# Kernel optimization log

Measured on AMD Instinct MI355X. Metric: run time of the kernel, lower is better.

The kernel has to match this reference:

```python
import jax, jax.numpy as jnp
import numpy as np

DIM = 1024
NUM_HEADS = 16
NUM_KV_HEADS = 4
HEAD_DIM = DIM // NUM_HEADS
KV_DIM = NUM_KV_HEADS * HEAD_DIM
PARTIAL_ROPE_DIM = 32
ROPE_BASE = 10000.0
LORA_RANK = 4
NUM_LORA_STEPS = 2
LORA_SCALE = 1.0
B, S = 2, 2048


def _rms_norm(x):
    eps = jnp.asarray(jnp.finfo(x.dtype).eps, x.dtype)
    return x * jax.lax.rsqrt(jnp.mean(x * x, axis=-1, keepdims=True) + eps)


def _rope_cos_sin(seq_len, dtype):
    half = PARTIAL_ROPE_DIM // 2
    inv_freq = 1.0 / (ROPE_BASE ** (jnp.arange(0, PARTIAL_ROPE_DIM, 2, dtype=jnp.float32) / PARTIAL_ROPE_DIM))
    t = jnp.arange(seq_len, dtype=jnp.float32)
    freqs = jnp.outer(t, inv_freq)  # [S, half]
    return jnp.cos(freqs).astype(dtype), jnp.sin(freqs).astype(dtype)


def _apply_rope_partial(x, cos, sin):
    # x: [B, H, S, D]; rotate first PARTIAL_ROPE_DIM dims, pass the rest.
    half = PARTIAL_ROPE_DIM // 2
    x1 = x[..., :half]
    x2 = x[..., half:PARTIAL_ROPE_DIM]
    xp = x[..., PARTIAL_ROPE_DIM:]
    c = cos[None, None, :, :]
    s = sin[None, None, :, :]
    return jnp.concatenate([x1 * c + x2 * s, -x1 * s + x2 * c, xp], axis=-1)


def setup_inputs() -> dict:
    key = jax.random.key(0)
    ks = jax.random.split(key, 12)
    std = 0.02
    return {
        "x": jax.random.normal(ks[0], (B, S, DIM), jnp.float32),
        "Wq": jax.random.normal(ks[1], (DIM, DIM), jnp.float32) * std,
        "Wk": jax.random.normal(ks[2], (KV_DIM, DIM), jnp.float32) * std,
        "Wv": jax.random.normal(ks[3], (KV_DIM, DIM), jnp.float32) * std,
        "Wproj": jax.random.normal(ks[4], (DIM, DIM), jnp.float32) * std,
        "q_gain": jnp.full((NUM_HEADS,), 1.0, jnp.float32),
        "lora_A_q": jax.random.normal(ks[5], (NUM_LORA_STEPS, LORA_RANK, DIM), jnp.float32) * std,
        "lora_B_q": jax.random.normal(ks[6], (NUM_LORA_STEPS, DIM, LORA_RANK), jnp.float32) * std,
        "lora_A_v": jax.random.normal(ks[7], (NUM_LORA_STEPS, LORA_RANK, DIM), jnp.float32) * std,
        "lora_B_v": jax.random.normal(ks[8], (NUM_LORA_STEPS, KV_DIM, LORA_RANK), jnp.float32) * std,
        "step_idx": 0,
    }


def reference(x, Wq, Wk, Wv, Wproj, q_gain, lora_A_q, lora_B_q, lora_A_v, lora_B_v, step_idx):
    bsz, seqlen, dim = x.shape
    q = x @ Wq.T
    v = x @ Wv.T
    if 0 <= step_idx < NUM_LORA_STEPS:
        q = q + LORA_SCALE * ((x @ lora_A_q[step_idx].T) @ lora_B_q[step_idx].T)
        v = v + LORA_SCALE * ((x @ lora_A_v[step_idx].T) @ lora_B_v[step_idx].T)
    k = x @ Wk.T

    q = q.reshape(bsz, seqlen, NUM_HEADS, HEAD_DIM).transpose(0, 2, 1, 3)      # [B,H,S,D]
    k = k.reshape(bsz, seqlen, NUM_KV_HEADS, HEAD_DIM).transpose(0, 2, 1, 3)   # [B,Hkv,S,D]
    v = v.reshape(bsz, seqlen, NUM_KV_HEADS, HEAD_DIM).transpose(0, 2, 1, 3)

    q = _rms_norm(q)
    k = _rms_norm(k)

    cos, sin = _rope_cos_sin(seqlen, q.dtype)
    q = _apply_rope_partial(q, cos, sin)
    k = _apply_rope_partial(k, cos, sin)

    q = q * q_gain.astype(q.dtype)[None, :, None, None]

    # GQA causal SDPA
    groups = NUM_HEADS // NUM_KV_HEADS
    qg = q.reshape(bsz, NUM_KV_HEADS, groups, seqlen, HEAD_DIM)
    scale = 1.0 / np.sqrt(HEAD_DIM)
    scores = jnp.einsum('bkgsd,bktd->bkgst', qg, k) * scale  # [B,Hkv,G,S,S]
    causal = jnp.tril(jnp.ones((seqlen, seqlen), bool))
    scores = jnp.where(causal[None, None, None], scores, jnp.asarray(-jnp.inf, scores.dtype))
    attn = jax.nn.softmax(scores, axis=-1)
    y = jnp.einsum('bkgst,bktd->bkgsd', attn, v)
    y = y.reshape(bsz, NUM_HEADS, seqlen, HEAD_DIM).transpose(0, 2, 1, 3).reshape(bsz, seqlen, dim)
    return y @ Wproj.T
```

## Files before the change

kernel.cpp:

```cpp
#include <hip/hip_runtime.h>
#include <hip/hip_bf16.h>
#include <stdint.h>

#define DIM 1024
#define NH 16
#define NKV 4
#define HD 64
#define SEQ 2048
#define BATCH 2
#define RANK 4
#define NSTEPS 2

#define XN      4194304
#define WQ_END  5242880
#define WK_END  5505024
#define WV_END  5767168
#define CVT_BLOCKS 6656
#define LORA_BLOCKS 1024

typedef unsigned short u16;
typedef unsigned int u32;
typedef __attribute__((ext_vector_type(8))) __bf16 bf16x8;
typedef __attribute__((ext_vector_type(4))) float f32x4;

__device__ __forceinline__ float bf2f(u16 v) {
    u32 u = ((u32)v) << 16;
    return __builtin_bit_cast(float, u);
}
__device__ __forceinline__ u16 f2bf(float f) {
    u32 u = __builtin_bit_cast(u32, f);
    u32 r = (u + 0x7fffu + ((u >> 16) & 1u)) >> 16;
    return (u16)r;
}
__device__ __forceinline__ u32 pk2(float a, float b) {
    return (u32)f2bf(a) | ((u32)f2bf(b) << 16);
}
__device__ __forceinline__ u32 pk2t(float a, float b) {
    return __builtin_amdgcn_perm(__builtin_bit_cast(u32, b),
                                 __builtin_bit_cast(u32, a), 0x07060302u);
}
__device__ __forceinline__ void glds16(const u16* g, u16* l) {
    __builtin_amdgcn_global_load_lds(
        (const __attribute__((address_space(1))) u32*)g,
        (__attribute__((address_space(3))) u32*)l, 16, 0, 0);
}

__global__ __launch_bounds__(256) void k_prep(
    const float* __restrict__ x, const float* __restrict__ Wq,
    const float* __restrict__ Wk, const float* __restrict__ Wv,
    const float* __restrict__ Wp, u16* __restrict__ dst,
    const float* __restrict__ Aq, const float* __restrict__ Av,
    const int* __restrict__ step_p, float* __restrict__ tq, float* __restrict__ tv)
{
    int bx = blockIdx.x;
    if (bx < CVT_BLOCKS) {
        int e = (bx * 256 + threadIdx.x) * 4;
        const float* src;
        if (e < XN)          src = x  + e;
        else if (e < WQ_END) src = Wq + (e - XN);
        else if (e < WK_END) src = Wk + (e - WQ_END);
        else if (e < WV_END) src = Wv + (e - WK_END);
        else                 src = Wp + (e - WV_END);
        float4 v = *(const float4*)src;
        *(uint2*)(dst + e) = make_uint2(pk2(v.x, v.y), pk2(v.z, v.w));
        return;
    }
    int wave = ((bx - CVT_BLOCKS) * 256 + threadIdx.x) >> 6;
    int lane = threadIdx.x & 63;
    int step = step_p[0];
    int valid = (step >= 0 && step < NSTEPS);
    int sc = valid ? step : 0;
    const float* xr = x + wave * DIM + lane * 16;
    float xf[16];
#pragma unroll
    for (int q = 0; q < 4; q++) {
        float4 v4 = *(const float4*)(xr + q * 4);
        xf[q * 4 + 0] = v4.x; xf[q * 4 + 1] = v4.y;
        xf[q * 4 + 2] = v4.z; xf[q * 4 + 3] = v4.w;
    }
    float sums[8];
#pragma unroll
    for (int j = 0; j < 8; j++) {
        const float* ar = (j < 4 ? Aq + sc * RANK * DIM + j * DIM
                                 : Av + sc * RANK * DIM + (j - 4) * DIM) + lane * 16;
        float s = 0.f;
#pragma unroll
        for (int q = 0; q < 4; q++) {
            float4 a4 = *(const float4*)(ar + q * 4);
            s += xf[q * 4 + 0] * a4.x + xf[q * 4 + 1] * a4.y
               + xf[q * 4 + 2] * a4.z + xf[q * 4 + 3] * a4.w;
        }
#pragma unroll
        for (int o = 32; o > 0; o >>= 1) s += __shfl_xor(s, o, 64);
        sums[j] = s;
    }
    if (!valid) {
#pragma unroll
        for (int j = 0; j < 8; j++) sums[j] = 0.f;
    }
    if (lane == 0) {
        tq[wave * 4 + 0] = sums[0]; tq[wave * 4 + 1] = sums[1];
        tq[wave * 4 + 2] = sums[2]; tq[wave * 4 + 3] = sums[3];
        tv[wave * 4 + 0] = sums[4]; tv[wave * 4 + 1] = sums[5];
        tv[wave * 4 + 2] = sums[6]; tv[wave * 4 + 3] = sums[7];
    }
}

__global__ __launch_bounds__(256) void k_gemm_qkv(
    const u16* __restrict__ A, const u16* __restrict__ B,
    u16* __restrict__ qkv, u16* __restrict__ vtb,
    const float* __restrict__ tq, const float* __restrict__ Bq,
    const float* __restrict__ tv, const float* __restrict__ Bv,
    const float* __restrict__ gain, const int* __restrict__ step_p)
{
    __shared__ __align__(16) u16 As[8192];
    __shared__ __align__(16) u16 Bs[8192];
    int bx = blockIdx.x;
    int xcd = bx & 7, o = bx >> 3;
    int bm = xcd * 4 + (o & 3);
    int bn = o >> 2;
    int t = threadIdx.x, lane = t & 63, w = t >> 6;
    int wy = w >> 1, wx = w & 1;
    int wb = t & ~63;
    int quad = lane >> 4, n16 = lane & 15;
    f32x4 acc[4][4];
#pragma unroll
    for (int i = 0; i < 4; i++)
#pragma unroll
        for (int j = 0; j < 4; j++) acc[i][j] = (f32x4){0.f, 0.f, 0.f, 0.f};

    int goff[4];
#pragma unroll
    for (int u = 0; u < 4; u++) {
        int idx = u * 256 + t;
        int grp = idx >> 6;
        int q_ = (idx >> 4) & 3, m = idx & 15;
        goff[u] = ((grp >> 1) * 16 + m) * DIM + (grp & 1) * 32 + q_ * 8;
    }
    const u16* Ab = A + bm * 128 * DIM;
    const u16* Bb = B + bn * 128 * DIM;

#pragma unroll 1
    for (int kb = 0; kb < 16; kb++) {
        int k0 = kb * 64;
        __syncthreads();
#pragma unroll
        for (int u = 0; u < 4; u++)
            glds16(Ab + goff[u] + k0, As + (u * 256 + wb) * 8);
#pragma unroll
        for (int u = 0; u < 4; u++)
            glds16(Bb + goff[u] + k0, Bs + (u * 256 + wb) * 8);
        __syncthreads();
#pragma unroll
        for (int c = 0; c < 2; c++) {
            bf16x8 af[4], bfr[4];
#pragma unroll
            for (int i = 0; i < 4; i++)
                af[i] = *(const bf16x8*)(As + (((wy * 4 + i) * 2 + c) * 64 + lane) * 8);
#pragma unroll
            for (int j = 0; j < 4; j++)
                bfr[j] = *(const bf16x8*)(Bs + (((wx * 4 + j) * 2 + c) * 64 + lane) * 8);
#pragma unroll
            for (int i = 0; i < 4; i++)
#pragma unroll
                for (int j = 0; j < 4; j++)
                    acc[i][j] = __builtin_amdgcn_mfma_f32_16x16x32_bf16(af[i], bfr[j], acc[i][j], 0, 0, 0);
        }
    }

    int step = step_p[0];
    int sc = (step >= 0 && step < NSTEPS) ? step : 0;
    int row_base = bm * 128 + wy * 64 + quad * 4;

    if (bn < 10) {
        bool isq = (bn < 8);
        int h2 = isq ? (bn * 2 + wx) : ((bn - 8) * 2 + wx);
        int colbase = isq ? (h2 * 64) : (1024 + h2 * 64);
        if (isq) {
            float4 B4[4];
#pragma unroll
            for (int j = 0; j < 4; j++)
                B4[j] = *(const float4*)(Bq + (sc * DIM + h2 * 64 + j * 16 + n16) * RANK);
#pragma unroll
            for (int i = 0; i < 4; i++)
#pragma unroll
                for (int r = 0; r < 4; r++) {
                    float4 t4 = *(const float4*)(tq + (row_base + i * 16 + r) * 4);
#pragma unroll
                    for (int j = 0; j < 4; j++)
                        acc[i][j][r] += t4.x * B4[j].x + t4.y * B4[j].y
                                      + t4.z * B4[j].z + t4.w * B4[j].w;
                }
        }
        float postmul = isq ? (gain[h2] * 0.125f * 1.4426950408889634f) : 1.f;
        float invf = exp2f(-(float)n16 * 0.8304820237218405f);
#pragma unroll
        for (int i = 0; i < 4; i++)
#pragma unroll
            for (int r = 0; r < 4; r++) {
                float s = acc[i][0][r] * acc[i][0][r] + acc[i][1][r] * acc[i][1][r]
                        + acc[i][2][r] * acc[i][2][r] + acc[i][3][r] * acc[i][3][r];
#pragma unroll
                for (int o2 = 1; o2 < 16; o2 <<= 1) s += __shfl_xor(s, o2, 64);
                float rr = rsqrtf(s * (1.f / 64.f) + 1.1920928955078125e-7f);
                int row = row_base + i * 16 + r;
                float v0 = acc[i][0][r] * rr, v1 = acc[i][1][r] * rr;
                float v2 = acc[i][2][r] * rr, v3 = acc[i][3][r] * rr;
                float ang = (float)(row & 2047) * invf;
                float cs = cosf(ang), sn = sinf(ang);
                float o0 = v0 * cs + v1 * sn;
                float o1 = -v0 * sn + v1 * cs;
                u16* dst = qkv + row * 1536 + colbase + n16;
                dst[0]  = f2bf(o0 * postmul);
                dst[16] = f2bf(o1 * postmul);
                dst[32] = f2bf(v2 * postmul);
                dst[48] = f2bf(v3 * postmul);
            }
    } else {
        int g = (bn - 10) * 2 + wx;
        float4 B4[4];
#pragma unroll
        for (int j = 0; j < 4; j++)
            B4[j] = *(const float4*)(Bv + (sc * (NKV * HD) + g * 64 + j * 16 + n16) * RANK);
#pragma unroll
        for (int i = 0; i < 4; i++) {
#pragma unroll
            for (int r = 0; r < 4; r++) {
                float4 t4 = *(const float4*)(tv + (row_base + i * 16 + r) * 4);
#pragma unroll
                for (int j = 0; j < 4; j++)
                    acc[i][j][r] += t4.x * B4[j].x + t4.y * B4[j].y
                                  + t4.z * B4[j].z + t4.w * B4[j].w;
            }
            int row0 = row_base + i * 16;
            int b = row0 >> 11, s0 = row0 & 2047;
#pragma unroll
            for (int j = 0; j < 4; j++) {
                int d = j * 16 + n16;
                uint2 pkv = make_uint2(pk2(acc[i][j][0], acc[i][j][1]),
                                       pk2(acc[i][j][2], acc[i][j][3]));
                *(uint2*)(vtb + ((b * NKV + g) * HD + d) * SEQ + s0) = pkv;
            }
        }
    }
}

__global__ __launch_bounds__(256) void k_gemm_proj(
    const u16* __restrict__ A, const u16* __restrict__ B,
    float* __restrict__ C)
{
    __shared__ __align__(16) u16 As[8192];
    __shared__ __align__(16) u16 Bs[4096];
    int bx = blockIdx.x;
    int bn = (bx & 7) * 2 + ((bx >> 3) & 1);
    int bm = bx >> 4;
    int t = threadIdx.x, lane = t & 63, w = t >> 6;
    int wy = w >> 1, wx = w & 1;
    int wb = t & ~63;
    f32x4 acc[4][2];
#pragma unroll
    for (int i = 0; i < 4; i++)
#pragma unroll
        for (int j = 0; j < 2; j++) acc[i][j] = (f32x4){0.f, 0.f, 0.f, 0.f};

    int goffA[4], goffB[2];
#pragma unroll
    for (int u = 0; u < 4; u++) {
        int idx = u * 256 + t;
        int grp = idx >> 6;
        int q_ = (idx >> 4) & 3, m = idx & 15;
        goffA[u] = ((grp >> 1) * 16 + m) * DIM + (grp & 1) * 32 + q_ * 8;
    }
#pragma unroll
    for (int u = 0; u < 2; u++) {
        int idx = u * 256 + t;
        int grp = idx >> 6;
        int q_ = (idx >> 4) & 3, m = idx & 15;
        goffB[u] = ((grp >> 1) * 16 + m) * DIM + (grp & 1) * 32 + q_ * 8;
    }
    const u16* Ab = A + bm * 128 * DIM;
    const u16* Bb = B + bn * 64 * DIM;

#pragma unroll 1
    for (int kb = 0; kb < 16; kb++) {
        int k0 = kb * 64;
        __syncthreads();
#pragma unroll
        for (int u = 0; u < 4; u++)
            glds16(Ab + goffA[u] + k0, As + (u * 256 + wb) * 8);
#pragma unroll
        for (int u = 0; u < 2; u++)
            glds16(Bb + goffB[u] + k0, Bs + (u * 256 + wb) * 8);
        __syncthreads();
#pragma unroll
        for (int c = 0; c < 2; c++) {
            bf16x8 af[4], bfr[2];
#pragma unroll
            for (int i = 0; i < 4; i++)
                af[i] = *(const bf16x8*)(As + (((wy * 4 + i) * 2 + c) * 64 + lane) * 8);
#pragma unroll
            for (int j = 0; j < 2; j++)
                bfr[j] = *(const bf16x8*)(Bs + (((wx * 2 + j) * 2 + c) * 64 + lane) * 8);
#pragma unroll
            for (int i = 0; i < 4; i++)
#pragma unroll
                for (int j = 0; j < 2; j++)
                    acc[i][j] = __builtin_amdgcn_mfma_f32_16x16x32_bf16(af[i], bfr[j], acc[i][j], 0, 0, 0);
        }
    }
    int quad = lane >> 4, n16 = lane & 15;
#pragma unroll
    for (int i = 0; i < 4; i++)
#pragma unroll
        for (int j = 0; j < 2; j++) {
            int col = bn * 64 + wx * 32 + j * 16 + n16;
#pragma unroll
            for (int r = 0; r < 4; r++) {
                int rowm = bm * 128 + wy * 64 + i * 16 + quad * 4 + r;
                C[rowm * DIM + col] = acc[i][j][r];
            }
        }
}

__global__ __launch_bounds__(256) void k_attn(
    const u16* __restrict__ qkv, const u16* __restrict__ vt,
    const float* __restrict__ gain, u16* __restrict__ y)
{
    __shared__ __align__(16) u16 kf[2][4096];
    __shared__ __align__(16) u16 vf[2][4096];
    __shared__ __align__(16) u16 pb[4][1024];
    int bx = blockIdx.x;
    int bgid = bx & 7, inner = bx >> 3;
    int b = bgid >> 2, g = bgid & 3;
    int h = g * 4 + (inner & 3);
    int qtsel = (inner >> 2) & 15;
    int t = threadIdx.x, lane = t & 63, w = t >> 6, wb = t & ~63;
    int quad = lane >> 4, n16 = lane & 15;
    float negM = -11.67f * fabsf(gain[h]);

    const u16* kbase = qkv + b * SEQ * 1536 + 1024 + g * HD;
    const u16* vbase = vt + (b * NKV + g) * HD * SEQ;

    int koff0, koff1, voff0, voff1;
    {
        int s0 = t, r0 = s0 >> 3, c0 = (s0 & 7) ^ (r0 & 7);
        koff0 = r0 * 1536 + c0 * 8;  voff0 = r0 * 2048 + c0 * 8;
        int s1 = 256 + t, r1 = s1 >> 3, c1 = (s1 & 7) ^ (r1 & 7);
        koff1 = r1 * 1536 + c1 * 8;  voff1 = r1 * 2048 + c1 * 8;
    }
    int swb = n16 & 7;
    int o0 = n16 * 8 + (quad ^ swb);
    int o1 = n16 * 8 + ((4 + quad) ^ swb);
    u16* pw = pb[w];

    f32x4 acc[4];
    float ps;
    bf16x8 qlo, qhi;
    int qrow;

    auto reset_acc = [&]() {
#pragma unroll
        for (int i = 0; i < 4; i++) acc[i] = (f32x4){0.f, 0.f, 0.f, 0.f};
        ps = 0.f;
    };
    auto load_q = [&](int qt) {
        qrow = qt * 64 + w * 16 + n16;
        const u16* qp = qkv + (b * SEQ + qrow) * 1536 + h * HD + quad * 8;
        qlo = *(const bf16x8*)qp;
        qhi = *(const bf16x8*)(qp + 32);
    };
    auto stage = [&](int kt, int p) {
        const u16* kp = kbase + kt * (64 * 1536);
        const u16* vp = vbase + kt * 64;
        glds16(kp + koff0, kf[p] + wb * 8);
        glds16(kp + koff1, kf[p] + (256 + wb) * 8);
        glds16(vp + voff0, vf[p] + wb * 8);
        glds16(vp + voff1, vf[p] + (256 + wb) * 8);
    };
    auto compute = [&](int kt, int p, bool diag) {
        f32x4 st[4];
#pragma unroll
        for (int nt = 0; nt < 4; nt++) {
            f32x4 sa = (f32x4){0.f, 0.f, 0.f, 0.f};
            sa = __builtin_amdgcn_mfma_f32_16x16x32_bf16(*(bf16x8*)(kf[p] + (nt * 128 + o0) * 8), qlo, sa, 0, 0, 0);
            sa = __builtin_amdgcn_mfma_f32_16x16x32_bf16(*(bf16x8*)(kf[p] + (nt * 128 + o1) * 8), qhi, sa, 0, 0, 0);
            st[nt] = sa;
        }
        float pr[4][4];
        if (diag) {
            int kb0 = kt * 64;
#pragma unroll
            for (int nt = 0; nt < 4; nt++)
#pragma unroll
                for (int r = 0; r < 4; r++) {
                    int key = kb0 + nt * 16 + quad * 4 + r;
                    float e = exp2f(st[nt][r] + negM);
                    e = (key > qrow) ? 0.f : e;
                    pr[nt][r] = e;
                    ps += e;
                }
        } else {
#pragma unroll
            for (int nt = 0; nt < 4; nt++)
#pragma unroll
                for (int r = 0; r < 4; r++) {
                    float e = exp2f(st[nt][r] + negM);
                    pr[nt][r] = e;
                    ps += e;
                }
        }
#pragma unroll
        for (int nt = 0; nt < 4; nt++) {
            u32 lo = pk2t(pr[nt][0], pr[nt][1]);
            u32 hi = pk2t(pr[nt][2], pr[nt][3]);
            int ck = nt >> 1;
            int qbk = (nt & 1) * 2 + (quad >> 1);
            int byteoff = (ck * 64 + qbk * 16 + n16) * 16 + (quad & 1) * 8;
            *(uint2*)((char*)pw + byteoff) = make_uint2(lo, hi);
        }
        asm volatile("s_waitcnt lgkmcnt(0)" ::: "memory");
#pragma unroll
        for (int ck = 0; ck < 2; ck++) {
            bf16x8 pfr = *(bf16x8*)(pw + (ck * 64 + lane) * 8);
            int oo = ck ? o1 : o0;
#pragma unroll
            for (int dt = 0; dt < 4; dt++)
                acc[dt] = __builtin_amdgcn_mfma_f32_16x16x32_bf16(*(bf16x8*)(vf[p] + (dt * 128 + oo) * 8), pfr, acc[dt], 0, 0, 0);
        }
        asm volatile("" ::: "memory");
    };
    auto run = [&](int kt0, int kt1, bool diag_last) {
        int p = 0;
        stage(kt0, 0);
#pragma unroll 1
        for (int kt = kt0; kt < kt1; kt++) {
            if (kt + 1 < kt1) {
                stage(kt + 1, p ^ 1);
                asm volatile("s_waitcnt vmcnt(4)" ::: "memory");
            } else {
                asm volatile("s_waitcnt vmcnt(0)" ::: "memory");
            }
            __builtin_amdgcn_s_barrier();
            compute(kt, p, diag_last && (kt == kt1 - 1));
            asm volatile("s_waitcnt lgkmcnt(0)" ::: "memory");
            __builtin_amdgcn_s_barrier();
            p ^= 1;
        }
    };
    auto finish = [&]() {
        float pt = ps + __shfl_xor(ps, 16, 64);
        pt += __shfl_xor(pt, 32, 64);
        float li = 1.f / pt;
#pragma unroll
        for (int dt = 0; dt < 4; dt++) {
            uint2 o = make_uint2(pk2(acc[dt][0] * li, acc[dt][1] * li),
                                 pk2(acc[dt][2] * li, acc[dt][3] * li));
            int d = dt * 16 + quad * 4;
            *(uint2*)(y + (b * SEQ + qrow) * DIM + h * HD + d) = o;
        }
    };

    load_q(qtsel);
    reset_acc();
    run(0, qtsel + 1, true);
    finish();
    load_q(31 - qtsel);
    reset_acc();
    run(0, 32 - qtsel, true);
    finish();
}

extern "C" void kernel_launch(void* const* d_in, const int* in_sizes, int n_in,
                              void* d_out, int out_size, void* d_ws, size_t ws_size,
                              hipStream_t stream)
{
    (void)in_sizes; (void)n_in; (void)out_size; (void)ws_size;
    const float* x     = (const float*)d_in[0];
    const float* Wq    = (const float*)d_in[1];
    const float* Wk    = (const float*)d_in[2];
    const float* Wv    = (const float*)d_in[3];
    const float* Wproj = (const float*)d_in[4];
    const float* qgain = (const float*)d_in[5];
    const float* Aq    = (const float*)d_in[6];
    const float* Bq    = (const float*)d_in[7];
    const float* Av    = (const float*)d_in[8];
    const float* Bv    = (const float*)d_in[9];
    const int*   step  = (const int*)d_in[10];

    char* ws = (char*)d_ws;
    u16* wsbf = (u16*)ws;
    u16* xb   = wsbf;
    u16* wf   = wsbf + XN;
    u16* wp   = wsbf + WV_END;
    u16* qkv  = (u16*)(ws + 13631488);
    float* tq = (float*)(ws + 26214400);
    float* tv = tq + 16384;
    u16* vt   = (u16*)(ws + 26607616);
    u16* y    = xb;

    k_prep<<<CVT_BLOCKS + LORA_BLOCKS, 256, 0, stream>>>(x, Wq, Wk, Wv, Wproj, wsbf,
                                                         Aq, Av, step, tq, tv);
    k_gemm_qkv<<<384, 256, 0, stream>>>(xb, wf, qkv, vt, tq, Bq, tv, Bv, qgain, step);
    k_attn<<<512, 256, 0, stream>>>(qkv, vt, qgain, y);
    k_gemm_proj<<<512, 256, 0, stream>>>(y, wp, (float*)d_out);
}
```

Before: 209.1 us.

## Double-buffer LDS tiles in QKV and proj GEMMs, raise MFMA wave priority in attention

Both GEMM kernels now use two LDS buffers, so the global-to-LDS load for the next K block is issued before computing on the current one, with one barrier per iteration instead of two. The attention kernel wraps its MFMA sections in s_setprio(1) so matrix work gets scheduling priority over other waves. Double buffering doubles LDS per block (64KB for the QKV GEMM), which may lower occupancy.

```diff
diff --git a/kernel.cpp b/kernel.cpp
--- a/kernel.cpp
+++ b/kernel.cpp
@@ -113,8 +113,8 @@
     const float* __restrict__ tv, const float* __restrict__ Bv,
     const float* __restrict__ gain, const int* __restrict__ step_p)
 {
-    __shared__ __align__(16) u16 As[8192];
-    __shared__ __align__(16) u16 Bs[8192];
+    __shared__ __align__(16) u16 As[2][8192];
+    __shared__ __align__(16) u16 Bs[2][8192];
     int bx = blockIdx.x;
     int xcd = bx & 7, o = bx >> 3;
     int bm = xcd * 4 + (o & 3);
@@ -140,33 +140,49 @@
     const u16* Ab = A + bm * 128 * DIM;
     const u16* Bb = B + bn * 128 * DIM;
 
-#pragma unroll 1
-    for (int kb = 0; kb < 16; kb++) {
+    auto stage = [&](int kb, int p) {
         int k0 = kb * 64;
-        __syncthreads();
 #pragma unroll
         for (int u = 0; u < 4; u++)
-            glds16(Ab + goff[u] + k0, As + (u * 256 + wb) * 8);
+            glds16(Ab + goff[u] + k0, As[p] + (u * 256 + wb) * 8);
 #pragma unroll
         for (int u = 0; u < 4; u++)
-            glds16(Bb + goff[u] + k0, Bs + (u * 256 + wb) * 8);
-        __syncthreads();
+            glds16(Bb + goff[u] + k0, Bs[p] + (u * 256 + wb) * 8);
+    };
+    auto compute = [&](int p) {
+        const u16* Asc = As[p];
+        const u16* Bsc = Bs[p];
 #pragma unroll
         for (int c = 0; c < 2; c++) {
             bf16x8 af[4], bfr[4];
 #pragma unroll
             for (int i = 0; i < 4; i++)
-                af[i] = *(const bf16x8*)(As + (((wy * 4 + i) * 2 + c) * 64 + lane) * 8);
+                af[i] = *(const bf16x8*)(Asc + (((wy * 4 + i) * 2 + c) * 64 + lane) * 8);
 #pragma unroll
             for (int j = 0; j < 4; j++)
-                bfr[j] = *(const bf16x8*)(Bs + (((wx * 4 + j) * 2 + c) * 64 + lane) * 8);
+                bfr[j] = *(const bf16x8*)(Bsc + (((wx * 4 + j) * 2 + c) * 64 + lane) * 8);
 #pragma unroll
             for (int i = 0; i < 4; i++)
 #pragma unroll
                 for (int j = 0; j < 4; j++)
                     acc[i][j] = __builtin_amdgcn_mfma_f32_16x16x32_bf16(af[i], bfr[j], acc[i][j], 0, 0, 0);
         }
-    }
+    };
+
+    stage(0, 0);
+    asm volatile("s_waitcnt vmcnt(0)" ::: "memory");
+    __builtin_amdgcn_s_barrier();
+    int cur = 0;
+#pragma unroll 1
+    for (int kb = 0; kb < 15; kb++) {
+        stage(kb + 1, cur ^ 1);
+        compute(cur);
+        asm volatile("s_waitcnt vmcnt(0)" ::: "memory");
+        __builtin_amdgcn_s_barrier();
+        cur ^= 1;
+    }
+    compute(cur);
+    __syncthreads();
 
     int step = step_p[0];
     int sc = (step >= 0 && step < NSTEPS) ? step : 0;
@@ -249,8 +265,8 @@
     const u16* __restrict__ A, const u16* __restrict__ B,
     float* __restrict__ C)
 {
-    __shared__ __align__(16) u16 As[8192];
-    __shared__ __align__(16) u16 Bs[4096];
+    __shared__ __align__(16) u16 As[2][8192];
+    __shared__ __align__(16) u16 Bs[2][4096];
     int bx = blockIdx.x;
     int bn = (bx & 7) * 2 + ((bx >> 3) & 1);
     int bm = bx >> 4;
@@ -281,33 +297,49 @@
     const u16* Ab = A + bm * 128 * DIM;
     const u16* Bb = B + bn * 64 * DIM;
 
-#pragma unroll 1
-    for (int kb = 0; kb < 16; kb++) {
+    auto stage = [&](int kb, int p) {
         int k0 = kb * 64;
-        __syncthreads();
 #pragma unroll
         for (int u = 0; u < 4; u++)
-            glds16(Ab + goffA[u] + k0, As + (u * 256 + wb) * 8);
+            glds16(Ab + goffA[u] + k0, As[p] + (u * 256 + wb) * 8);
 #pragma unroll
         for (int u = 0; u < 2; u++)
-            glds16(Bb + goffB[u] + k0, Bs + (u * 256 + wb) * 8);
-        __syncthreads();
+            glds16(Bb + goffB[u] + k0, Bs[p] + (u * 256 + wb) * 8);
+    };
+    auto compute = [&](int p) {
+        const u16* Asc = As[p];
+        const u16* Bsc = Bs[p];
 #pragma unroll
         for (int c = 0; c < 2; c++) {
             bf16x8 af[4], bfr[2];
 #pragma unroll
             for (int i = 0; i < 4; i++)
-                af[i] = *(const bf16x8*)(As + (((wy * 4 + i) * 2 + c) * 64 + lane) * 8);
+                af[i] = *(const bf16x8*)(Asc + (((wy * 4 + i) * 2 + c) * 64 + lane) * 8);
 #pragma unroll
             for (int j = 0; j < 2; j++)
-                bfr[j] = *(const bf16x8*)(Bs + (((wx * 2 + j) * 2 + c) * 64 + lane) * 8);
+                bfr[j] = *(const bf16x8*)(Bsc + (((wx * 2 + j) * 2 + c) * 64 + lane) * 8);
 #pragma unroll
             for (int i = 0; i < 4; i++)
 #pragma unroll
                 for (int j = 0; j < 2; j++)
                     acc[i][j] = __builtin_amdgcn_mfma_f32_16x16x32_bf16(af[i], bfr[j], acc[i][j], 0, 0, 0);
         }
-    }
+    };
+
+    stage(0, 0);
+    asm volatile("s_waitcnt vmcnt(0)" ::: "memory");
+    __builtin_amdgcn_s_barrier();
+    int cur = 0;
+#pragma unroll 1
+    for (int kb = 0; kb < 15; kb++) {
+        stage(kb + 1, cur ^ 1);
+        compute(cur);
+        asm volatile("s_waitcnt vmcnt(0)" ::: "memory");
+        __builtin_amdgcn_s_barrier();
+        cur ^= 1;
+    }
+    compute(cur);
+
     int quad = lane >> 4, n16 = lane & 15;
 #pragma unroll
     for (int i = 0; i < 4; i++)
@@ -379,6 +411,7 @@
     };
     auto compute = [&](int kt, int p, bool diag) {
         f32x4 st[4];
+        __builtin_amdgcn_s_setprio(1);
 #pragma unroll
         for (int nt = 0; nt < 4; nt++) {
             f32x4 sa = (f32x4){0.f, 0.f, 0.f, 0.f};
@@ -386,6 +419,7 @@
             sa = __builtin_amdgcn_mfma_f32_16x16x32_bf16(*(bf16x8*)(kf[p] + (nt * 128 + o1) * 8), qhi, sa, 0, 0, 0);
             st[nt] = sa;
         }
+        __builtin_amdgcn_s_setprio(0);
         float pr[4][4];
         if (diag) {
             int kb0 = kt * 64;
@@ -419,6 +453,7 @@
             *(uint2*)((char*)pw + byteoff) = make_uint2(lo, hi);
         }
         asm volatile("s_waitcnt lgkmcnt(0)" ::: "memory");
+        __builtin_amdgcn_s_setprio(1);
 #pragma unroll
         for (int ck = 0; ck < 2; ck++) {
             bf16x8 pfr = *(bf16x8*)(pw + (ck * 64 + lane) * 8);
@@ -427,6 +462,7 @@
             for (int dt = 0; dt < 4; dt++)
                 acc[dt] = __builtin_amdgcn_mfma_f32_16x16x32_bf16(*(bf16x8*)(vf[p] + (dt * 128 + oo) * 8), pfr, acc[dt], 0, 0, 0);
         }
+        __builtin_amdgcn_s_setprio(0);
         asm volatile("" ::: "memory");
     };
     auto run = [&](int kt0, int kt1, bool diag_last) {
```

After: 248.6 us. +18.9%, slower.

## Process paired query tiles in one KV sweep to share K/V staging

Applied to the files above, without the earlier changes.

The attention block previously handled its two balanced query tiles (qtsel and 31-qtsel) in two separate passes over the key/value tiles, each restaging K and V into LDS. Now it keeps two accumulator sets and makes a single pass, applying each staged K/V tile to both query tiles while the shorter one is still within range. This removes the redundant global-to-LDS loads and barriers for the overlapping prefix. The cost is higher register pressure from the doubled accumulators and Q fragments, which may lower occupancy. It also adds s_setprio around the MFMA sections to favor matrix-instruction issue.

```diff
diff --git a/kernel.cpp b/kernel.cpp
--- a/kernel.cpp
+++ b/kernel.cpp
@@ -353,22 +353,25 @@
     int o1 = n16 * 8 + ((4 + quad) ^ swb);
     u16* pw = pb[w];
 
-    f32x4 acc[4];
-    float ps;
-    bf16x8 qlo, qhi;
-    int qrow;
-
-    auto reset_acc = [&]() {
-#pragma unroll
-        for (int i = 0; i < 4; i++) acc[i] = (f32x4){0.f, 0.f, 0.f, 0.f};
-        ps = 0.f;
-    };
-    auto load_q = [&](int qt) {
-        qrow = qt * 64 + w * 16 + n16;
-        const u16* qp = qkv + (b * SEQ + qrow) * 1536 + h * HD + quad * 8;
-        qlo = *(const bf16x8*)qp;
-        qhi = *(const bf16x8*)(qp + 32);
-    };
+    f32x4 accA[4], accB[4];
+    float psA = 0.f, psB = 0.f;
+#pragma unroll
+    for (int i = 0; i < 4; i++) {
+        accA[i] = (f32x4){0.f, 0.f, 0.f, 0.f};
+        accB[i] = (f32x4){0.f, 0.f, 0.f, 0.f};
+    }
+    int qrowA = qtsel * 64 + w * 16 + n16;
+    int qrowB = (31 - qtsel) * 64 + w * 16 + n16;
+    bf16x8 qloA, qhiA, qloB, qhiB;
+    {
+        const u16* qpA = qkv + (b * SEQ + qrowA) * 1536 + h * HD + quad * 8;
+        qloA = *(const bf16x8*)qpA;
+        qhiA = *(const bf16x8*)(qpA + 32);
+        const u16* qpB = qkv + (b * SEQ + qrowB) * 1536 + h * HD + quad * 8;
+        qloB = *(const bf16x8*)qpB;
+        qhiB = *(const bf16x8*)(qpB + 32);
+    }
+
     auto stage = [&](int kt, int p) {
         const u16* kp = kbase + kt * (64 * 1536);
         const u16* vp = vbase + kt * 64;
@@ -377,8 +380,10 @@
         glds16(vp + voff0, vf[p] + wb * 8);
         glds16(vp + voff1, vf[p] + (256 + wb) * 8);
     };
-    auto compute = [&](int kt, int p, bool diag) {
+    auto tilecomp = [&](f32x4* acc, float& ps, bf16x8 qlo, bf16x8 qhi,
+                        int qrow, int kt, int p, bool diag) {
         f32x4 st[4];
+        __builtin_amdgcn_s_setprio(1);
 #pragma unroll
         for (int nt = 0; nt < 4; nt++) {
             f32x4 sa = (f32x4){0.f, 0.f, 0.f, 0.f};
@@ -386,6 +391,7 @@
             sa = __builtin_amdgcn_mfma_f32_16x16x32_bf16(*(bf16x8*)(kf[p] + (nt * 128 + o1) * 8), qhi, sa, 0, 0, 0);
             st[nt] = sa;
         }
+        __builtin_amdgcn_s_setprio(0);
         float pr[4][4];
         if (diag) {
             int kb0 = kt * 64;
@@ -419,6 +425,7 @@
             *(uint2*)((char*)pw + byteoff) = make_uint2(lo, hi);
         }
         asm volatile("s_waitcnt lgkmcnt(0)" ::: "memory");
+        __builtin_amdgcn_s_setprio(1);
 #pragma unroll
         for (int ck = 0; ck < 2; ck++) {
             bf16x8 pfr = *(bf16x8*)(pw + (ck * 64 + lane) * 8);
@@ -427,27 +434,10 @@
             for (int dt = 0; dt < 4; dt++)
                 acc[dt] = __builtin_amdgcn_mfma_f32_16x16x32_bf16(*(bf16x8*)(vf[p] + (dt * 128 + oo) * 8), pfr, acc[dt], 0, 0, 0);
         }
+        __builtin_amdgcn_s_setprio(0);
         asm volatile("" ::: "memory");
     };
-    auto run = [&](int kt0, int kt1, bool diag_last) {
-        int p = 0;
-        stage(kt0, 0);
-#pragma unroll 1
-        for (int kt = kt0; kt < kt1; kt++) {
-            if (kt + 1 < kt1) {
-                stage(kt + 1, p ^ 1);
-                asm volatile("s_waitcnt vmcnt(4)" ::: "memory");
-            } else {
-                asm volatile("s_waitcnt vmcnt(0)" ::: "memory");
-            }
-            __builtin_amdgcn_s_barrier();
-            compute(kt, p, diag_last && (kt == kt1 - 1));
-            asm volatile("s_waitcnt lgkmcnt(0)" ::: "memory");
-            __builtin_amdgcn_s_barrier();
-            p ^= 1;
-        }
-    };
-    auto finish = [&]() {
+    auto finish = [&](f32x4* acc, float ps, int qrow) {
         float pt = ps + __shfl_xor(ps, 16, 64);
         pt += __shfl_xor(pt, 32, 64);
         float li = 1.f / pt;
@@ -460,14 +450,27 @@
         }
     };
 
-    load_q(qtsel);
-    reset_acc();
-    run(0, qtsel + 1, true);
-    finish();
-    load_q(31 - qtsel);
-    reset_acc();
-    run(0, 32 - qtsel, true);
-    finish();
+    int ktEnd = 32 - qtsel;
+    int p = 0;
+    stage(0, 0);
+#pragma unroll 1
+    for (int kt = 0; kt < ktEnd; kt++) {
+        if (kt + 1 < ktEnd) {
+            stage(kt + 1, p ^ 1);
+            asm volatile("s_waitcnt vmcnt(4)" ::: "memory");
+        } else {
+            asm volatile("s_waitcnt vmcnt(0)" ::: "memory");
+        }
+        __builtin_amdgcn_s_barrier();
+        if (kt <= qtsel)
+            tilecomp(accA, psA, qloA, qhiA, qrowA, kt, p, kt == qtsel);
+        tilecomp(accB, psB, qloB, qhiB, qrowB, kt, p, kt == ktEnd - 1);
+        asm volatile("s_waitcnt lgkmcnt(0)" ::: "memory");
+        __builtin_amdgcn_s_barrier();
+        p ^= 1;
+    }
+    finish(accA, psA, qrowA);
+    finish(accB, psB, qrowB);
 }
 
 extern "C" void kernel_launch(void* const* d_in, const int* in_sizes, int n_in,
```

Measured after the change: 209.1 us. Within noise of the previous version (-0.0%).
